# Optimization experiments

Measured on AMD Instinct MI355X. Metric: run time of the kernel, lower is better.

## Reference

```python
import jax, jax.numpy as jnp
import numpy as np

N = 100000      # nodes
E = 1600000     # edges (before self-loops)
F_IN = 128      # num_feats
H = 128         # dim_hidden
C = 64          # num_classes
EPS = 1e-5      # BatchNorm eps
SLOPE = 0.2     # LeakyReLU negative slope (PyG GATConv default)


def setup_inputs() -> dict:
    key = jax.random.key(0)
    ks = jax.random.split(key, 8)
    x = jax.random.normal(ks[0], (N, F_IN), jnp.float32)
    edge_index = jax.random.randint(ks[1], (2, E), 0, N, dtype=jnp.int32)
    W0 = jax.random.normal(ks[2], (F_IN, H), jnp.float32) * (1.0 / np.sqrt(F_IN))
    a_src0 = jax.random.normal(ks[3], (H,), jnp.float32) * 0.1
    a_dst0 = jax.random.normal(ks[4], (H,), jnp.float32) * 0.1
    W1 = jax.random.normal(ks[5], (H, C), jnp.float32) * (1.0 / np.sqrt(H))
    a_src1 = jax.random.normal(ks[6], (C,), jnp.float32) * 0.1
    a_dst1 = jax.random.normal(ks[7], (C,), jnp.float32) * 0.1
    return {
        "x": x, "edge_index": edge_index,
        "W0": W0, "a_src0": a_src0, "a_dst0": a_dst0,
        "g0": jnp.ones((H,), jnp.float32), "b0": jnp.zeros((H,), jnp.float32),
        "W1": W1, "a_src1": a_src1, "a_dst1": a_dst1,
        "g1": jnp.ones((C,), jnp.float32), "b1": jnp.zeros((C,), jnp.float32),
    }


def _gat_conv(x, src, dst, W, a_s, a_d):
    # x: [N, d_in]; src/dst: [E'] (self-loops included). heads=1, bias=False.
    h = x @ W                                   # [N, d_out]
    s = h @ a_s                                 # [N] alpha_src per node
    d = h @ a_d                                 # [N] alpha_dst per node
    logits = jax.nn.leaky_relu(s[src] + d[dst], SLOPE)   # [E']
    # segment softmax over incoming edges of each dst node
    m = jax.ops.segment_max(logits, dst, num_segments=N)
    w = jnp.exp(logits - m[dst])
    denom = jax.ops.segment_sum(w, dst, num_segments=N)
    coef = w / denom[dst]                       # [E']
    return jax.ops.segment_sum(coef[:, None] * h[src], dst, num_segments=N)


def _batch_norm(x, g, b):
    mu = jnp.mean(x, axis=0)
    var = jnp.var(x, axis=0)
    return (x - mu) * jax.lax.rsqrt(var + EPS) * g + b


def reference(x, edge_index, W0, a_src0, a_dst0, g0, b0, W1, a_src1, a_dst1, g1, b1):
    loops = jnp.arange(N, dtype=edge_index.dtype)
    src = jnp.concatenate([edge_index[0], loops])
    dst = jnp.concatenate([edge_index[1], loops])
    h = _gat_conv(x, src, dst, W0, a_src0, a_dst0)
    h = jax.nn.relu(_batch_norm(h, g0, b0))
    h = _gat_conv(h, src, dst, W1, a_src1, a_dst1)
    return jax.nn.relu(_batch_norm(h, g1, b1))
```

## Files before the change

kernel.cpp:

```cpp
#include <hip/hip_runtime.h>
#include <hip/hip_bf16.h>
#include <cmath>

#define BN_EPS 1e-5f
#define SLOPE 0.2f
#define BCAP 6144

typedef __attribute__((ext_vector_type(8))) short bf16x8;
typedef __attribute__((ext_vector_type(4))) float f32x4;

__device__ __forceinline__ float lrelu(float x) { return x >= 0.f ? x : SLOPE * x; }
__device__ __forceinline__ float bfl(unsigned u) { return __uint_as_float(u << 16); }
__device__ __forceinline__ float bfh(unsigned u) { return __uint_as_float(u & 0xffff0000u); }
__device__ __forceinline__ float bf2f(unsigned short u) { return __uint_as_float((unsigned)u << 16); }
__device__ __forceinline__ unsigned short f2bf(float f) {
    __hip_bfloat16 h = __float2bfloat16(f);
    return *reinterpret_cast<unsigned short*>(&h);
}

__global__ __launch_bounds__(512) void k_bucket(const int* __restrict__ ei, int E, int n,
                                                int nbk, int* __restrict__ gcnt,
                                                int2* __restrict__ bbuf) {
    __shared__ int h[512], off[512];
    int t = threadIdx.x;
    for (int i = t; i < nbk; i += 512) h[i] = 0;
    __syncthreads();
    int base = blockIdx.x * 8192;
    int tot = E + n;
    int srcv[16], dstv[16], rnk[16];
#pragma unroll
    for (int k = 0; k < 16; ++k) {
        int i = base + k * 512 + t;
        dstv[k] = -1;
        if (i < tot) {
            int s_, d_;
            if (i < E) { s_ = ei[i]; d_ = ei[E + i]; }
            else       { s_ = i - E; d_ = s_; }
            srcv[k] = s_; dstv[k] = d_;
            rnk[k] = atomicAdd(&h[d_ >> 8], 1);
        }
    }
    __syncthreads();
    for (int i = t; i < nbk; i += 512)
        if (h[i]) off[i] = atomicAdd(&gcnt[i], h[i]);
    __syncthreads();
#pragma unroll
    for (int k = 0; k < 16; ++k) {
        int d_ = dstv[k];
        if (d_ >= 0) {
            int b = d_ >> 8;
            bbuf[(size_t)b * BCAP + off[b] + rnk[k]] = make_int2(srcv[k], d_);
        }
    }
}

__global__ __launch_bounds__(512) void k_bscan(const int* __restrict__ gcnt,
                                               int* __restrict__ gbase, int nbk) {
    __shared__ int tmp[512];
    int t = threadIdx.x;
    int v = (t < nbk) ? gcnt[t] : 0;
    tmp[t] = v;
    __syncthreads();
    for (int off = 1; off < 512; off <<= 1) {
        int a = (t >= off) ? tmp[t - off] : 0;
        __syncthreads();
        tmp[t] += a;
        __syncthreads();
    }
    int ex = tmp[t] - v;
    if (t < nbk) gbase[t] = ex;
    if (t == nbk - 1) gbase[nbk] = tmp[t];
}

__global__ __launch_bounds__(256) void k_csr2(const int2* __restrict__ bbuf,
                                              const int* __restrict__ gcnt,
                                              const int* __restrict__ gbase,
                                              int* __restrict__ rowp, int* __restrict__ csr,
                                              int n, int nbk) {
    __shared__ int cnt[256], scn[256];
    int b = blockIdx.x;
    int t = threadIdx.x;
    int cntb = gcnt[b];
    int gb = gbase[b];
    const int2* bb = bbuf + (size_t)b * BCAP;
    int node0 = b << 8;
    cnt[t] = 0;
    __syncthreads();
    for (int i = t; i < cntb; i += 256)
        atomicAdd(&cnt[bb[i].y & 255], 1);
    __syncthreads();
    int v = cnt[t];
    scn[t] = v;
    __syncthreads();
    for (int off = 1; off < 256; off <<= 1) {
        int a = (t >= off) ? scn[t - off] : 0;
        __syncthreads();
        scn[t] += a;
        __syncthreads();
    }
    int ex = scn[t] - v;
    if (node0 + t < n) rowp[node0 + t] = gb + ex;
    if (b == nbk - 1 && t == 0) rowp[n] = gb + cntb;
    cnt[t] = ex;
    __syncthreads();
    for (int i = t; i < cntb; i += 256) {
        int2 e = bb[i];
        int pos = atomicAdd(&cnt[e.y & 255], 1);
        csr[gb + pos] = e.x;
    }
}

__global__ void k_packw2(const float* __restrict__ W0, const float* __restrict__ W1,
                         unsigned short* __restrict__ Wp0, unsigned short* __restrict__ Wp1) {
    int idx = blockIdx.x * 256 + threadIdx.x;
    if (idx < 128 * 128) {
        int k = idx >> 7, nG = idx & 127;
        int nt = nG >> 4, nn = nG & 15, ks = k >> 5, g = (k >> 3) & 3, j = k & 7;
        Wp0[(((nt * 4 + ks) * 64) + g * 16 + nn) * 8 + j] = f2bf(W0[idx]);
    } else {
        int i2 = idx - 128 * 128;
        if (i2 < 128 * 64) {
            int k = i2 >> 6, nG = i2 & 63;
            int nt = nG >> 4, nn = nG & 15, ks = k >> 5, g = (k >> 3) & 3, j = k & 7;
            Wp1[(((nt * 4 + ks) * 64) + g * 16 + nn) * 8 + j] = f2bf(W1[i2]);
        }
    }
}

template <int CD, bool BN_IN, bool XBF>
__global__ __launch_bounds__(256) void k_gemm_mfma(
    const void* __restrict__ Xv, const unsigned short* __restrict__ Wp,
    const float* __restrict__ bnsums, const float* __restrict__ gg,
    const float* __restrict__ bb, const float* __restrict__ a_s,
    const float* __restrict__ a_d, unsigned short* __restrict__ hb,
    float* __restrict__ s_out, float* __restrict__ d_out, int n) {
    constexpr int NT = CD / 16;
    const float* Xf = (const float*)Xv;
    const unsigned short* Xh = (const unsigned short*)Xv;
    __shared__ unsigned short wl[128 * CD];
    __shared__ float sc[128], sh[128];
    int t = threadIdx.x;
    for (int i = t * 8; i < 128 * CD; i += 2048)
        *(uint4*)&wl[i] = *(const uint4*)&Wp[i];
    if constexpr (BN_IN) {
        if (t < 128) {
            float invn = 1.f / (float)n;
            float mu = bnsums[t] * invn;
            float var = bnsums[128 + t] * invn - mu * mu;
            float s = gg[t] * rsqrtf(var + BN_EPS);
            sc[t] = s;
            sh[t] = bb[t] - mu * s;
        }
    }
    __syncthreads();
    int w = t >> 6, l = t & 63;
    int m = l & 15, g = l >> 4;
    int r0 = blockIdx.x * 64;
    int row = r0 + w * 16 + m;
    bool rv = row < n;
    bf16x8 af[4];
#pragma unroll
    for (int ks = 0; ks < 4; ++ks) {
        int c0 = ks * 32 + g * 8;
        float xv[8];
        if constexpr (XBF) {
            uint4 u = make_uint4(0, 0, 0, 0);
            if (rv) u = *(const uint4*)&Xh[(size_t)row * 128 + c0];
            unsigned uu[4] = {u.x, u.y, u.z, u.w};
#pragma unroll
            for (int q = 0; q < 4; ++q) { xv[2 * q] = bfl(uu[q]); xv[2 * q + 1] = bfh(uu[q]); }
        } else {
            float4 x0 = make_float4(0.f, 0.f, 0.f, 0.f), x1 = x0;
            if (rv) {
                x0 = *(const float4*)&Xf[(size_t)row * 128 + c0];
                x1 = *(const float4*)&Xf[(size_t)row * 128 + c0 + 4];
            }
            xv[0] = x0.x; xv[1] = x0.y; xv[2] = x0.z; xv[3] = x0.w;
            xv[4] = x1.x; xv[5] = x1.y; xv[6] = x1.z; xv[7] = x1.w;
        }
        bf16x8 a;
#pragma unroll
        for (int j = 0; j < 8; ++j) {
            float v = xv[j];
            if constexpr (BN_IN) v = fmaxf(0.f, v * sc[c0 + j] + sh[c0 + j]);
            a[j] = (short)f2bf(v);
        }
        af[ks] = a;
    }
    f32x4 acc[NT];
#pragma unroll
    for (int i = 0; i < NT; ++i) acc[i] = (f32x4){0.f, 0.f, 0.f, 0.f};
#pragma unroll
    for (int ks = 0; ks < 4; ++ks) {
#pragma unroll
        for (int nt = 0; nt < NT; ++nt) {
            bf16x8 bfr = *(bf16x8*)&wl[(((nt * 4 + ks) * 64) + l) * 8];
            acc[nt] = __builtin_amdgcn_mfma_f32_16x16x32_bf16(af[ks], bfr, acc[nt], 0, 0, 0);
        }
    }
    float ps[4] = {0.f, 0.f, 0.f, 0.f}, pd[4] = {0.f, 0.f, 0.f, 0.f};
#pragma unroll
    for (int nt = 0; nt < NT; ++nt) {
        float as = a_s[nt * 16 + m], ad = a_d[nt * 16 + m];
#pragma unroll
        for (int r = 0; r < 4; ++r) {
            ps[r] += acc[nt][r] * as;
            pd[r] += acc[nt][r] * ad;
        }
    }
#pragma unroll
    for (int off = 1; off < 16; off <<= 1) {
#pragma unroll
        for (int r = 0; r < 4; ++r) {
            ps[r] += __shfl_xor(ps[r], off);
            pd[r] += __shfl_xor(pd[r], off);
        }
    }
    __syncthreads();
    unsigned short* ot = wl;
#pragma unroll
    for (int nt = 0; nt < NT; ++nt) {
#pragma unroll
        for (int r = 0; r < 4; ++r)
            ot[(w * 16 + g * 4 + r) * CD + nt * 16 + m] = f2bf(acc[nt][r]);
    }
    if (m == 0) {
        int orow = r0 + w * 16 + g * 4;
#pragma unroll
        for (int r = 0; r < 4; ++r) {
            if (orow + r < n) { s_out[orow + r] = ps[r]; d_out[orow + r] = pd[r]; }
        }
    }
    __syncthreads();
    constexpr int CPR = CD / 8;
    for (int c = t; c < 64 * CPR; c += 256) {
        int rr = c / CPR, cc = c % CPR;
        if (r0 + rr < n)
            *(uint4*)&hb[(size_t)(r0 + rr) * CD + cc * 8] = *(uint4*)&ot[rr * CD + cc * 8];
    }
}

template <int DIM, bool OUT_BF>
__global__ __launch_bounds__(256) void k_agg(
    const unsigned short* __restrict__ hb, const float* __restrict__ s,
    const float* __restrict__ d, const int* __restrict__ rowp,
    const int* __restrict__ csr, void* __restrict__ outv, int n) {
    constexpr int LPE = DIM / 8;
    int gid = blockIdx.x * blockDim.x + threadIdx.x;
    int wid = gid / LPE;
    int ll = gid & (LPE - 1);
    if (wid >= n) return;
    int beg = rowp[wid], end = rowp[wid + 1];
    float dv = d[wid];
    const unsigned short* hbl = hb + ll * 8;
    float acc[8] = {};
    float denom = 0.f;
    int e = beg;
    if (e + 3 < end) {
        int lim = end - 1;
        int i0 = csr[e], i1 = csr[e + 1], i2 = csr[e + 2], i3 = csr[e + 3];
        float s0 = s[i0], s1 = s[i1], s2 = s[i2], s3 = s[i3];
        while (true) {
            int en = e + 4;
            int c0 = en < lim ? en : lim;
            int c1 = en + 1 < lim ? en + 1 : lim;
            int c2 = en + 2 < lim ? en + 2 : lim;
            int c3 = en + 3 < lim ? en + 3 : lim;
            int j0 = csr[c0], j1 = csr[c1], j2 = csr[c2], j3 = csr[c3];
            float t0 = s[j0], t1 = s[j1], t2 = s[j2], t3 = s[j3];
            uint4 p0 = *(const uint4*)&hbl[(size_t)i0 * DIM];
            uint4 p1 = *(const uint4*)&hbl[(size_t)i1 * DIM];
            uint4 p2 = *(const uint4*)&hbl[(size_t)i2 * DIM];
            uint4 p3 = *(const uint4*)&hbl[(size_t)i3 * DIM];
            float w0 = __expf(lrelu(s0 + dv));
            float w1 = __expf(lrelu(s1 + dv));
            float w2 = __expf(lrelu(s2 + dv));
            float w3 = __expf(lrelu(s3 + dv));
            denom += (w0 + w1) + (w2 + w3);
            unsigned a0[4] = {p0.x, p0.y, p0.z, p0.w};
            unsigned a1[4] = {p1.x, p1.y, p1.z, p1.w};
            unsigned a2[4] = {p2.x, p2.y, p2.z, p2.w};
            unsigned a3[4] = {p3.x, p3.y, p3.z, p3.w};
#pragma unroll
            for (int q = 0; q < 4; ++q) {
                acc[2 * q]     += w0 * bfl(a0[q]) + w1 * bfl(a1[q]) + w2 * bfl(a2[q]) + w3 * bfl(a3[q]);
                acc[2 * q + 1] += w0 * bfh(a0[q]) + w1 * bfh(a1[q]) + w2 * bfh(a2[q]) + w3 * bfh(a3[q]);
            }
            e = en;
            if (e + 3 >= end) break;
            i0 = j0; i1 = j1; i2 = j2; i3 = j3;
            s0 = t0; s1 = t1; s2 = t2; s3 = t3;
        }
    }
    for (; e < end; ++e) {
        int i0 = csr[e];
        float w0 = __expf(lrelu(s[i0] + dv));
        uint4 p0 = *(const uint4*)&hbl[(size_t)i0 * DIM];
        unsigned a0[4] = {p0.x, p0.y, p0.z, p0.w};
        denom += w0;
#pragma unroll
        for (int q = 0; q < 4; ++q) {
            acc[2 * q]     += w0 * bfl(a0[q]);
            acc[2 * q + 1] += w0 * bfh(a0[q]);
        }
    }
    float inv = 1.f / denom;
    if constexpr (OUT_BF) {
        unsigned u[4];
#pragma unroll
        for (int q = 0; q < 4; ++q)
            u[q] = (unsigned)f2bf(acc[2 * q] * inv) |
                   ((unsigned)f2bf(acc[2 * q + 1] * inv) << 16);
        *(uint4*)((unsigned short*)outv + (size_t)wid * DIM + ll * 8) =
            make_uint4(u[0], u[1], u[2], u[3]);
    } else {
        float* orow = (float*)outv + (size_t)wid * DIM + ll * 8;
        *(float4*)&orow[0] = make_float4(acc[0] * inv, acc[1] * inv, acc[2] * inv, acc[3] * inv);
        *(float4*)&orow[4] = make_float4(acc[4] * inv, acc[5] * inv, acc[6] * inv, acc[7] * inv);
    }
}

template <int CD, bool XBF>
__global__ void k_bn_stats(const void* __restrict__ xv, float* __restrict__ sums, int n) {
    const float* xf = (const float*)xv;
    const unsigned short* xh = (const unsigned short*)xv;
    constexpr int RPB = 256 / CD;
    int t = threadIdx.x;
    int c = t & (CD - 1);
    int rl = t / CD;
    float s = 0.f, sq = 0.f;
    for (int r = blockIdx.x * RPB + rl; r < n; r += gridDim.x * RPB) {
        float v = XBF ? bf2f(xh[(size_t)r * CD + c]) : xf[(size_t)r * CD + c];
        s += v;
        sq += v * v;
    }
    __shared__ float ls[256], lq[256];
    ls[t] = s; lq[t] = sq;
    __syncthreads();
    if (t < CD) {
#pragma unroll
        for (int j = 1; j < RPB; ++j) { s += ls[t + j * CD]; sq += lq[t + j * CD]; }
        atomicAdd(&sums[c], s);
        atomicAdd(&sums[CD + c], sq);
    }
}

template <int CD>
__global__ void k_bn_apply(const float* __restrict__ x, const float* __restrict__ sums,
                           const float* __restrict__ g, const float* __restrict__ b,
                           float* __restrict__ out, int n) {
    size_t i = (size_t)blockIdx.x * blockDim.x + threadIdx.x;
    size_t tot = (size_t)n * CD;
    if (i >= tot) return;
    int c = (int)(i & (CD - 1));
    float invn = 1.f / (float)n;
    float mu = sums[c] * invn;
    float var = sums[CD + c] * invn - mu * mu;
    float v = (x[i] - mu) * rsqrtf(var + BN_EPS) * g[c] + b[c];
    out[i] = fmaxf(v, 0.f);
}

extern "C" void kernel_launch(void* const* d_in, const int* in_sizes, int n_in,
                              void* d_out, int out_size, void* d_ws, size_t ws_size,
                              hipStream_t stream) {
    const float* x   = (const float*)d_in[0];
    const int*   ei  = (const int*)  d_in[1];
    const float* W0  = (const float*)d_in[2];
    const float* as0 = (const float*)d_in[3];
    const float* ad0 = (const float*)d_in[4];
    const float* g0  = (const float*)d_in[5];
    const float* b0  = (const float*)d_in[6];
    const float* W1  = (const float*)d_in[7];
    const float* as1 = (const float*)d_in[8];
    const float* ad1 = (const float*)d_in[9];
    const float* g1  = (const float*)d_in[10];
    const float* b1  = (const float*)d_in[11];
    float* out = (float*)d_out;

    const int N_ = in_sizes[0] / 128;
    const int E_ = in_sizes[1] / 2;
    const int TOT = E_ + N_;
    const int nbk = (N_ + 255) >> 8;

    char* p = (char*)d_ws;
    unsigned short* hb   = (unsigned short*)p; p += (size_t)N_ * 128 * 2;
    unsigned short* aggB = (unsigned short*)p; p += (size_t)N_ * 128 * 2;
    float* agg1 = (float*)p;                   p += (size_t)N_ * 64 * 4;
    int2* bbuf  = (int2*)p;                    p += (size_t)nbk * BCAP * 8;
    float* s0   = (float*)p;                   p += (size_t)N_ * 4;
    float* d0   = (float*)p;                   p += (size_t)N_ * 4;
    float* bns0 = (float*)p;                   p += 256 * 4;
    float* bns1 = (float*)p;                   p += 128 * 4;
    int* gcnt   = (int*)p;                     p += 512 * 4;
    int* gbase  = (int*)p;                     p += 514 * 4;
    int* rowp   = (int*)p;                     p += (size_t)(N_ + 2) * 4;
    int* csr    = (int*)p;                     p += (size_t)TOT * 4;
    unsigned short* Wp0 = (unsigned short*)p;  p += 128 * 128 * 2;
    unsigned short* Wp1 = (unsigned short*)p;  p += 128 * 64 * 2;

    hipMemsetAsync(gcnt, 0, 512 * 4, stream);
    hipMemsetAsync(bns0, 0, 384 * 4, stream);

    const int gemmBlocks = (N_ + 63) / 64;
    const int aggBlocks128 = (N_ + 15) / 16;
    const int aggBlocks64  = (N_ + 31) / 32;
    const int ebBlocks = (TOT + 8191) / 8192;

    k_packw2<<<96, 256, 0, stream>>>(W0, W1, Wp0, Wp1);
    k_gemm_mfma<128, false, false><<<gemmBlocks, 256, 0, stream>>>(
        x, Wp0, nullptr, nullptr, nullptr, as0, ad0, hb, s0, d0, N_);

    k_bucket<<<ebBlocks, 512, 0, stream>>>(ei, E_, N_, nbk, gcnt, bbuf);
    k_bscan<<<1, 512, 0, stream>>>(gcnt, gbase, nbk);
    k_csr2<<<nbk, 256, 0, stream>>>(bbuf, gcnt, gbase, rowp, csr, N_, nbk);

    k_agg<128, true><<<aggBlocks128, 256, 0, stream>>>(hb, s0, d0, rowp, csr, aggB, N_);
    k_bn_stats<128, true><<<256, 256, 0, stream>>>(aggB, bns0, N_);

    k_gemm_mfma<64, true, true><<<gemmBlocks, 256, 0, stream>>>(
        aggB, Wp1, bns0, g0, b0, as1, ad1, hb, s0, d0, N_);
    k_agg<64, false><<<aggBlocks64, 256, 0, stream>>>(hb, s0, d0, rowp, csr, agg1, N_);
    k_bn_stats<64, false><<<256, 256, 0, stream>>>(agg1, bns1, N_);
    k_bn_apply<64><<<(int)(((size_t)N_ * 64 + 255) / 256), 256, 0, stream>>>(
        agg1, bns1, g1, b1, out, N_);
}
```

Baseline: 369.8 us.

## Sort nodes by in-degree for aggregation and fold memsets and bucket scan

Builds a degree histogram in the CSR kernel, scans it, and produces a permutation that groups destination nodes by in-degree. Both aggregation kernels then process nodes in that order, so lanes in a wavefront handle similar-length edge lists and waste less time on divergence. It also removes the two memset calls by zeroing counters inside the weight-pack kernel, and replaces the separate bucket scan kernel with a per-block reduction inside the CSR kernel. The cost is two extra small kernels, an indirection through perm in aggregation, and output writes that are no longer in node order.

```diff
diff --git a/kernel.cpp b/kernel.cpp
--- a/kernel.cpp
+++ b/kernel.cpp
@@ -18,101 +18,18 @@
     return *reinterpret_cast<unsigned short*>(&h);
 }
 
-__global__ __launch_bounds__(512) void k_bucket(const int* __restrict__ ei, int E, int n,
-                                                int nbk, int* __restrict__ gcnt,
-                                                int2* __restrict__ bbuf) {
-    __shared__ int h[512], off[512];
-    int t = threadIdx.x;
-    for (int i = t; i < nbk; i += 512) h[i] = 0;
-    __syncthreads();
-    int base = blockIdx.x * 8192;
-    int tot = E + n;
-    int srcv[16], dstv[16], rnk[16];
-#pragma unroll
-    for (int k = 0; k < 16; ++k) {
-        int i = base + k * 512 + t;
-        dstv[k] = -1;
-        if (i < tot) {
-            int s_, d_;
-            if (i < E) { s_ = ei[i]; d_ = ei[E + i]; }
-            else       { s_ = i - E; d_ = s_; }
-            srcv[k] = s_; dstv[k] = d_;
-            rnk[k] = atomicAdd(&h[d_ >> 8], 1);
-        }
-    }
-    __syncthreads();
-    for (int i = t; i < nbk; i += 512)
-        if (h[i]) off[i] = atomicAdd(&gcnt[i], h[i]);
-    __syncthreads();
-#pragma unroll
-    for (int k = 0; k < 16; ++k) {
-        int d_ = dstv[k];
-        if (d_ >= 0) {
-            int b = d_ >> 8;
-            bbuf[(size_t)b * BCAP + off[b] + rnk[k]] = make_int2(srcv[k], d_);
-        }
-    }
-}
-
-__global__ __launch_bounds__(512) void k_bscan(const int* __restrict__ gcnt,
-                                               int* __restrict__ gbase, int nbk) {
-    __shared__ int tmp[512];
-    int t = threadIdx.x;
-    int v = (t < nbk) ? gcnt[t] : 0;
-    tmp[t] = v;
-    __syncthreads();
-    for (int off = 1; off < 512; off <<= 1) {
-        int a = (t >= off) ? tmp[t - off] : 0;
-        __syncthreads();
-        tmp[t] += a;
-        __syncthreads();
-    }
-    int ex = tmp[t] - v;
-    if (t < nbk) gbase[t] = ex;
-    if (t == nbk - 1) gbase[nbk] = tmp[t];
-}
-
-__global__ __launch_bounds__(256) void k_csr2(const int2* __restrict__ bbuf,
-                                              const int* __restrict__ gcnt,
-                                              const int* __restrict__ gbase,
-                                              int* __restrict__ rowp, int* __restrict__ csr,
-                                              int n, int nbk) {
-    __shared__ int cnt[256], scn[256];
-    int b = blockIdx.x;
-    int t = threadIdx.x;
-    int cntb = gcnt[b];
-    int gb = gbase[b];
-    const int2* bb = bbuf + (size_t)b * BCAP;
-    int node0 = b << 8;
-    cnt[t] = 0;
-    __syncthreads();
-    for (int i = t; i < cntb; i += 256)
-        atomicAdd(&cnt[bb[i].y & 255], 1);
-    __syncthreads();
-    int v = cnt[t];
-    scn[t] = v;
-    __syncthreads();
-    for (int off = 1; off < 256; off <<= 1) {
-        int a = (t >= off) ? scn[t - off] : 0;
-        __syncthreads();
-        scn[t] += a;
-        __syncthreads();
-    }
-    int ex = scn[t] - v;
-    if (node0 + t < n) rowp[node0 + t] = gb + ex;
-    if (b == nbk - 1 && t == 0) rowp[n] = gb + cntb;
-    cnt[t] = ex;
-    __syncthreads();
-    for (int i = t; i < cntb; i += 256) {
-        int2 e = bb[i];
-        int pos = atomicAdd(&cnt[e.y & 255], 1);
-        csr[gb + pos] = e.x;
-    }
-}
-
 __global__ void k_packw2(const float* __restrict__ W0, const float* __restrict__ W1,
-                         unsigned short* __restrict__ Wp0, unsigned short* __restrict__ Wp1) {
-    int idx = blockIdx.x * 256 + threadIdx.x;
+                         unsigned short* __restrict__ Wp0, unsigned short* __restrict__ Wp1,
+                         int* __restrict__ gcnt, int* __restrict__ dhist,
+                         int* __restrict__ dcur, float* __restrict__ bns) {
+    int t = threadIdx.x;
+    if (blockIdx.x == 0) {
+        for (int i = t; i < 512; i += 256) gcnt[i] = 0;
+        dhist[t] = 0;
+        dcur[t] = 0;
+        if (t < 384) bns[t] = 0.f;
+    }
+    int idx = blockIdx.x * 256 + t;
     if (idx < 128 * 128) {
         int k = idx >> 7, nG = idx & 127;
         int nt = nG >> 4, nn = nG & 15, ks = k >> 5, g = (k >> 3) & 3, j = k & 7;
@@ -125,6 +42,128 @@
             Wp1[(((nt * 4 + ks) * 64) + g * 16 + nn) * 8 + j] = f2bf(W1[i2]);
         }
     }
+}
+
+__global__ __launch_bounds__(512) void k_bucket(const int* __restrict__ ei, int E, int n,
+                                                int nbk, int* __restrict__ gcnt,
+                                                int2* __restrict__ bbuf) {
+    __shared__ int h[512], off[512];
+    int t = threadIdx.x;
+    for (int i = t; i < nbk; i += 512) h[i] = 0;
+    __syncthreads();
+    int base = blockIdx.x * 8192;
+    int tot = E + n;
+    int srcv[16], dstv[16], rnk[16];
+#pragma unroll
+    for (int k = 0; k < 16; ++k) {
+        int i = base + k * 512 + t;
+        dstv[k] = -1;
+        if (i < tot) {
+            int s_, d_;
+            if (i < E) { s_ = ei[i]; d_ = ei[E + i]; }
+            else       { s_ = i - E; d_ = s_; }
+            srcv[k] = s_; dstv[k] = d_;
+            rnk[k] = atomicAdd(&h[d_ >> 8], 1);
+        }
+    }
+    __syncthreads();
+    for (int i = t; i < nbk; i += 512)
+        if (h[i]) off[i] = atomicAdd(&gcnt[i], h[i]);
+    __syncthreads();
+#pragma unroll
+    for (int k = 0; k < 16; ++k) {
+        int d_ = dstv[k];
+        if (d_ >= 0) {
+            int b = d_ >> 8;
+            bbuf[(size_t)b * BCAP + off[b] + rnk[k]] = make_int2(srcv[k], d_);
+        }
+    }
+}
+
+__global__ __launch_bounds__(256) void k_csr2(const int2* __restrict__ bbuf,
+                                              const int* __restrict__ gcnt,
+                                              int* __restrict__ rowp, int* __restrict__ csr,
+                                              int* __restrict__ dhist, int n, int nbk) {
+    __shared__ int cnt[256], scn[256];
+    int b = blockIdx.x;
+    int t = threadIdx.x;
+    int a = 0;
+    for (int i = t; i < b; i += 256) a += gcnt[i];
+    scn[t] = a;
+    __syncthreads();
+    for (int off = 128; off; off >>= 1) {
+        if (t < off) scn[t] += scn[t + off];
+        __syncthreads();
+    }
+    int gb = scn[0];
+    int cntb = gcnt[b];
+    const int2* bb = bbuf + (size_t)b * BCAP;
+    int node0 = b << 8;
+    __syncthreads();
+    cnt[t] = 0;
+    __syncthreads();
+    for (int i = t; i < cntb; i += 256)
+        atomicAdd(&cnt[bb[i].y & 255], 1);
+    __syncthreads();
+    int v = cnt[t];
+    scn[t] = v;
+    __syncthreads();
+    for (int off = 1; off < 256; off <<= 1) {
+        int a2 = (t >= off) ? scn[t - off] : 0;
+        __syncthreads();
+        scn[t] += a2;
+        __syncthreads();
+    }
+    int ex = scn[t] - v;
+    if (node0 + t < n) {
+        rowp[node0 + t] = gb + ex;
+        atomicAdd(&dhist[v < 255 ? v : 255], 1);
+    }
+    if (b == nbk - 1 && t == 0) rowp[n] = gb + cntb;
+    cnt[t] = ex;
+    __syncthreads();
+    for (int i = t; i < cntb; i += 256) {
+        int2 e = bb[i];
+        int pos = atomicAdd(&cnt[e.y & 255], 1);
+        csr[gb + pos] = e.x;
+    }
+}
+
+__global__ __launch_bounds__(256) void k_dscan(const int* __restrict__ dhist,
+                                               int* __restrict__ dbase) {
+    __shared__ int tmp[256];
+    int t = threadIdx.x;
+    int v = dhist[t];
+    tmp[t] = v;
+    __syncthreads();
+    for (int off = 1; off < 256; off <<= 1) {
+        int a = (t >= off) ? tmp[t - off] : 0;
+        __syncthreads();
+        tmp[t] += a;
+        __syncthreads();
+    }
+    dbase[t] = tmp[t] - v;
+}
+
+__global__ __launch_bounds__(256) void k_dperm(const int* __restrict__ rowp,
+                                               const int* __restrict__ dbase,
+                                               int* __restrict__ dcur,
+                                               int* __restrict__ perm, int n) {
+    __shared__ int h[256], off[256];
+    int t = threadIdx.x;
+    h[t] = 0;
+    __syncthreads();
+    int i = blockIdx.x * 256 + t;
+    int bin = -1, rnk = 0;
+    if (i < n) {
+        int deg = rowp[i + 1] - rowp[i];
+        bin = deg < 255 ? deg : 255;
+        rnk = atomicAdd(&h[bin], 1);
+    }
+    __syncthreads();
+    if (h[t]) off[t] = atomicAdd(&dcur[t], h[t]);
+    __syncthreads();
+    if (bin >= 0) perm[dbase[bin] + off[bin] + rnk] = i;
 }
 
 template <int CD, bool BN_IN, bool XBF>
@@ -244,12 +283,14 @@
 __global__ __launch_bounds__(256) void k_agg(
     const unsigned short* __restrict__ hb, const float* __restrict__ s,
     const float* __restrict__ d, const int* __restrict__ rowp,
-    const int* __restrict__ csr, void* __restrict__ outv, int n) {
+    const int* __restrict__ csr, const int* __restrict__ perm,
+    void* __restrict__ outv, int n) {
     constexpr int LPE = DIM / 8;
     int gid = blockIdx.x * blockDim.x + threadIdx.x;
-    int wid = gid / LPE;
+    int grp = gid / LPE;
     int ll = gid & (LPE - 1);
-    if (wid >= n) return;
+    if (grp >= n) return;
+    int wid = perm[grp];
     int beg = rowp[wid], end = rowp[wid + 1];
     float dv = d[wid];
     const unsigned short* hbl = hb + ll * 8;
@@ -389,37 +430,41 @@
     int2* bbuf  = (int2*)p;                    p += (size_t)nbk * BCAP * 8;
     float* s0   = (float*)p;                   p += (size_t)N_ * 4;
     float* d0   = (float*)p;                   p += (size_t)N_ * 4;
-    float* bns0 = (float*)p;                   p += 256 * 4;
-    float* bns1 = (float*)p;                   p += 128 * 4;
+    float* bns  = (float*)p;                   p += 384 * 4;
     int* gcnt   = (int*)p;                     p += 512 * 4;
-    int* gbase  = (int*)p;                     p += 514 * 4;
+    int* dhist  = (int*)p;                     p += 256 * 4;
+    int* dbase  = (int*)p;                     p += 256 * 4;
+    int* dcur   = (int*)p;                     p += 256 * 4;
     int* rowp   = (int*)p;                     p += (size_t)(N_ + 2) * 4;
     int* csr    = (int*)p;                     p += (size_t)TOT * 4;
+    int* perm   = (int*)p;                     p += (size_t)N_ * 4;
     unsigned short* Wp0 = (unsigned short*)p;  p += 128 * 128 * 2;
     unsigned short* Wp1 = (unsigned short*)p;  p += 128 * 64 * 2;
 
-    hipMemsetAsync(gcnt, 0, 512 * 4, stream);
-    hipMemsetAsync(bns0, 0, 384 * 4, stream);
+    float* bns0 = bns;
+    float* bns1 = bns + 256;
 
     const int gemmBlocks = (N_ + 63) / 64;
     const int aggBlocks128 = (N_ + 15) / 16;
     const int aggBlocks64  = (N_ + 31) / 32;
     const int ebBlocks = (TOT + 8191) / 8192;
-
-    k_packw2<<<96, 256, 0, stream>>>(W0, W1, Wp0, Wp1);
+    const int nodeBlocks = (N_ + 255) / 256;
+
+    k_packw2<<<96, 256, 0, stream>>>(W0, W1, Wp0, Wp1, gcnt, dhist, dcur, bns);
     k_gemm_mfma<128, false, false><<<gemmBlocks, 256, 0, stream>>>(
         x, Wp0, nullptr, nullptr, nullptr, as0, ad0, hb, s0, d0, N_);
 
     k_bucket<<<ebBlocks, 512, 0, stream>>>(ei, E_, N_, nbk, gcnt, bbuf);
-    k_bscan<<<1, 512, 0, stream>>>(gcnt, gbase, nbk);
-    k_csr2<<<nbk, 256, 0, stream>>>(bbuf, gcnt, gbase, rowp, csr, N_, nbk);
-
-    k_agg<128, true><<<aggBlocks128, 256, 0, stream>>>(hb, s0, d0, rowp, csr, aggB, N_);
+    k_csr2<<<nbk, 256, 0, stream>>>(bbuf, gcnt, rowp, csr, dhist, N_, nbk);
+    k_dscan<<<1, 256, 0, stream>>>(dhist, dbase);
+    k_dperm<<<nodeBlocks, 256, 0, stream>>>(rowp, dbase, dcur, perm, N_);
+
+    k_agg<128, true><<<aggBlocks128, 256, 0, stream>>>(hb, s0, d0, rowp, csr, perm, aggB, N_);
     k_bn_stats<128, true><<<256, 256, 0, stream>>>(aggB, bns0, N_);
 
     k_gemm_mfma<64, true, true><<<gemmBlocks, 256, 0, stream>>>(
         aggB, Wp1, bns0, g0, b0, as1, ad1, hb, s0, d0, N_);
-    k_agg<64, false><<<aggBlocks64, 256, 0, stream>>>(hb, s0, d0, rowp, csr, agg1, N_);
+    k_agg<64, false><<<aggBlocks64, 256, 0, stream>>>(hb, s0, d0, rowp, csr, perm, agg1, N_);
     k_bn_stats<64, false><<<256, 256, 0, stream>>>(agg1, bns1, N_);
     k_bn_apply<64><<<(int)(((size_t)N_ * 64 + 255) / 256), 256, 0, stream>>>(
         agg1, bns1, g1, b1, out, N_);
```

Result: slower. 650.9 us (+76.0%).
